# Kernel optimization log

Hardware: AMD Instinct MI355X
Metric: run time of the kernel (lower is better)

The kernel has to match this reference:

```python
import jax, jax.numpy as jnp
import numpy as np

FACTOR = 2  # StyleGAN upsample factor
K1D = jnp.array([1.0, 4.0, 6.0, 4.0, 1.0], dtype=jnp.float32)
# StyleGAN upfirdn padding for upsample: p = kw - factor = 3
# pad0 = (p+1)//2 + factor - 1 = 3 ; pad1 = p//2 = 1 (+1 extra trailing zero
# because lhs_dilation gives length 2D-1 while zero-insertion gives 2D)
PAD0, PAD1 = 3, 2


def _upfir_axis(x, k1d, axis):
    """Zero-insert (factor 2) + 5-tap FIR along one spatial axis, depthwise.

    x: [N, C, D, H, W]; axis in {2, 3, 4}.
    """
    C = x.shape[1]
    kshape = [1, 1, 1]
    kshape[axis - 2] = k1d.shape[0]
    kernel = jnp.broadcast_to(k1d.reshape(kshape), (C, 1) + tuple(kshape))
    dil = [1, 1, 1]
    dil[axis - 2] = FACTOR
    pad = [(0, 0)] * 3
    pad[axis - 2] = (PAD0, PAD1)
    return jax.lax.conv_general_dilated(
        x, kernel.astype(x.dtype),
        window_strides=(1, 1, 1), padding=pad, lhs_dilation=dil,
        dimension_numbers=('NCDHW', 'OIDHW', 'NCDHW'),
        feature_group_count=C)


def setup_inputs() -> dict:
    key = jax.random.key(0)
    x = jax.random.normal(key, (4, 32, 48, 48, 48), dtype=jnp.float32)
    return {"x": x}


def reference(x):
    # normalize so kernel sums to 1, then apply gain factor per axis so the
    # total gain is factor**3 (StyleGAN: k = k/sum(k) * gain * factor**ndim,
    # split evenly across the 3 separable passes -> factor per axis)
    k = (K1D / K1D.sum() * FACTOR).astype(x.dtype)
    for ax in (2, 3, 4):  # D, H, W
        x = _upfir_axis(x, k, ax)
    return x  # [N, C, 2D, 2H, 2W]
```

## Files before the change

### kernel.cpp

```cpp
#include <hip/hip_runtime.h>


#define IN_D 48
#define IN_H 48
#define IN_W 48
#define NC   128
#define TD   8
#define THI  8
#define NTX  24
#define NTY  16
#define NTHREADS (NTX * NTY)
#define LZ (TD + 2)
#define LY (THI + 2)
#define LXP 52
#define NROWS (LZ * LY)

__device__ __forceinline__ float4 f4_even(float4 a, float4 b) {
    return make_float4(0.5f * (a.x + b.x), 0.5f * (a.y + b.y),
                       0.5f * (a.z + b.z), 0.5f * (a.w + b.w));
}
__device__ __forceinline__ float4 f4_odd(float4 a, float4 b, float4 c) {
    return make_float4(0.125f * (a.x + c.x) + 0.75f * b.x,
                       0.125f * (a.y + c.y) + 0.75f * b.y,
                       0.125f * (a.z + c.z) + 0.75f * b.z,
                       0.125f * (a.w + c.w) + 0.75f * b.w);
}

__global__ __launch_bounds__(NTHREADS)
void upfir3d_kernel(const float* __restrict__ in,
                    float* __restrict__ out) {
    __shared__ float lds[NROWS * LXP];

    const int tx = threadIdx.x;
    const int ty = threadIdx.y;
    const int bh = blockIdx.x;
    const int dz = blockIdx.y;
    const int nc = blockIdx.z;

    const int ih0 = bh * THI;
    const int id0 = dz * TD;
    const float* inb = in + (size_t)nc * (IN_D * IN_H * IN_W);

    const int tid = ty * NTX + tx;

    if (tid < 2 * NROWS) {
        int row = tid >> 1;
        int col = (tid & 1) ? 49 : 0;
        lds[row * LXP + col] = 0.0f;
    }

    {
        const int q = tid % 12;
        for (int row = tid / 12; row < NROWS; row += NTHREADS / 12) {
            int z  = row / LY;
            int y  = row - z * LY;
            int gd = id0 - 1 + z;
            int gh = ih0 - 1 + y;
            float4 v = make_float4(0.f, 0.f, 0.f, 0.f);
            if ((unsigned)gd < (unsigned)IN_D && (unsigned)gh < (unsigned)IN_H) {
                v = *reinterpret_cast<const float4*>(
                        inb + ((size_t)gd * IN_H + gh) * IN_W + 4 * q);
            }
            float* dst = &lds[row * LXP + 1 + 4 * q];
            dst[0] = v.x; dst[1] = v.y; dst[2] = v.z; dst[3] = v.w;
        }
    }
    __syncthreads();

    const int p   = ty & 1;
    const float wga = p ? 0.125f : 0.5f;
    const float wgb = p ? 0.75f  : 0.5f;
    const float wgc = p ? 0.125f : 0.0f;
    const int yy0 = ty >> 1;
    const int cx  = 2 * tx;

    auto whpart = [&](int z) -> float4 {
        const float* pp = &lds[(z * LY + yy0) * LXP + cx];
        float4 q4 = make_float4(0.f, 0.f, 0.f, 0.f);
#pragma unroll
        for (int dy = 0; dy < 3; ++dy) {
            const float wt = (dy == 0) ? wga : (dy == 1) ? wgb : wgc;
            float2 a = *reinterpret_cast<const float2*>(pp + dy * LXP);
            float2 b = *reinterpret_cast<const float2*>(pp + dy * LXP + 2);
            float w0 = 0.5f   * (a.x + a.y);
            float w1 = 0.125f * (a.x + b.x) + 0.75f * a.y;
            float w2 = 0.5f   * (a.y + b.x);
            float w3 = 0.125f * (a.y + b.y) + 0.75f * b.x;
            q4.x += wt * w0; q4.y += wt * w1;
            q4.z += wt * w2; q4.w += wt * w3;
        }
        return q4;
    };

    float4 qm = whpart(0);
    float4 qc = whpart(1);

    const int OH = 2 * IN_H, OW = 2 * IN_W;
    const int orow = 2 * ih0 + ty;
    float* ob = out + (size_t)nc * (2 * IN_D * OH * OW)
                    + (size_t)orow * OW + 4 * tx;
    const size_t plane = (size_t)OH * OW;

#pragma unroll
    for (int d = 0; d < TD; ++d) {
        float4 qp = whpart(d + 2);
        const int od = 2 * (id0 + d);

        *reinterpret_cast<float4*>(ob + (size_t)od * plane)       = f4_even(qm, qc);
        *reinterpret_cast<float4*>(ob + (size_t)(od + 1) * plane) = f4_odd(qm, qc, qp);

        qm = qc;
        qc = qp;
    }
}

extern "C" void kernel_launch(void* const* d_in, const int* in_sizes, int n_in,
                              void* d_out, int out_size, void* d_ws, size_t ws_size,
                              hipStream_t stream) {
    const float* x = (const float*)d_in[0];
    float* out = (float*)d_out;

    dim3 grid(IN_H / THI, IN_D / TD, NC);
    dim3 block(NTX, NTY, 1);
    upfir3d_kernel<<<grid, block, 0, stream>>>(x, out);
}
```

Measured before the change: 480.5 us.

## Tile full H extent per block with register-blocked rows and shallower depth tile

Each block now covers the full 48-row H extent and a 4-deep D slab, instead of an 8x8 H-by-D tile. Each thread computes 6 row groups held in register arrays, and the H halo rows are no longer reloaded by neighbouring blocks. The grid shrinks to 12x128 blocks, the LDS footprint grows to about 62KB, and register pressure rises. Output addressing moves to 32-bit unsigned offsets, which cuts address arithmetic but relies on per-batch offsets fitting in 32 bits.

```diff
diff --git a/kernel.cpp b/kernel.cpp
--- a/kernel.cpp
+++ b/kernel.cpp
@@ -5,15 +5,16 @@
 #define IN_H 48
 #define IN_W 48
 #define NC   128
-#define TD   8
-#define THI  8
+#define TD   4
 #define NTX  24
 #define NTY  16
 #define NTHREADS (NTX * NTY)
-#define LZ (TD + 2)
-#define LY (THI + 2)
+#define LZ  (TD + 2)
+#define LYS 50
 #define LXP 52
-#define NROWS (LZ * LY)
+#define NR  6
+#define OWD 96
+#define PLANE (96 * 96)
 
 __device__ __forceinline__ float4 f4_even(float4 a, float4 b) {
     return make_float4(0.5f * (a.x + b.x), 0.5f * (a.y + b.y),
@@ -29,88 +30,95 @@
 __global__ __launch_bounds__(NTHREADS)
 void upfir3d_kernel(const float* __restrict__ in,
                     float* __restrict__ out) {
-    __shared__ float lds[NROWS * LXP];
+    __shared__ float lds[LZ * LYS * LXP];
 
     const int tx = threadIdx.x;
     const int ty = threadIdx.y;
-    const int bh = blockIdx.x;
-    const int dz = blockIdx.y;
-    const int nc = blockIdx.z;
-
-    const int ih0 = bh * THI;
+    const int dz = blockIdx.x;
+    const int nc = blockIdx.y;
     const int id0 = dz * TD;
     const float* inb = in + (size_t)nc * (IN_D * IN_H * IN_W);
-
     const int tid = ty * NTX + tx;
 
-    if (tid < 2 * NROWS) {
-        int row = tid >> 1;
-        int col = (tid & 1) ? 49 : 0;
-        lds[row * LXP + col] = 0.0f;
+    for (int idx = tid; idx < LZ * 2 * LXP; idx += NTHREADS) {
+        int z   = idx / (2 * LXP);
+        int rem = idx - z * (2 * LXP);
+        int y   = (rem < LXP) ? 0 : (LYS - 1);
+        int col = (rem < LXP) ? rem : rem - LXP;
+        lds[(z * LYS + y) * LXP + col] = 0.0f;
     }
-
-    {
-        const int q = tid % 12;
-        for (int row = tid / 12; row < NROWS; row += NTHREADS / 12) {
-            int z  = row / LY;
-            int y  = row - z * LY;
-            int gd = id0 - 1 + z;
-            int gh = ih0 - 1 + y;
-            float4 v = make_float4(0.f, 0.f, 0.f, 0.f);
-            if ((unsigned)gd < (unsigned)IN_D && (unsigned)gh < (unsigned)IN_H) {
-                v = *reinterpret_cast<const float4*>(
-                        inb + ((size_t)gd * IN_H + gh) * IN_W + 4 * q);
-            }
-            float* dst = &lds[row * LXP + 1 + 4 * q];
-            dst[0] = v.x; dst[1] = v.y; dst[2] = v.z; dst[3] = v.w;
-        }
+    for (int idx = tid; idx < LZ * IN_H * 2; idx += NTHREADS) {
+        int z   = idx / (IN_H * 2);
+        int rem = idx - z * (IN_H * 2);
+        int y   = 1 + (rem >> 1);
+        int col = (rem & 1) ? 49 : 0;
+        lds[(z * LYS + y) * LXP + col] = 0.0f;
+    }
+    for (int idx = tid; idx < LZ * IN_H * 12; idx += NTHREADS) {
+        int q  = idx % 12;
+        int rf = idx / 12;
+        int z  = rf / IN_H;
+        int y  = rf - z * IN_H;
+        int gd = id0 - 1 + z;
+        float4 v = make_float4(0.f, 0.f, 0.f, 0.f);
+        if ((unsigned)gd < (unsigned)IN_D)
+            v = *reinterpret_cast<const float4*>(
+                    inb + ((size_t)gd * IN_H + y) * IN_W + 4 * q);
+        float* dst = &lds[(z * LYS + 1 + y) * LXP + 1 + 4 * q];
+        dst[0] = v.x; dst[1] = v.y; dst[2] = v.z; dst[3] = v.w;
     }
     __syncthreads();
 
-    const int p   = ty & 1;
+    const int p = ty & 1;
     const float wga = p ? 0.125f : 0.5f;
     const float wgb = p ? 0.75f  : 0.5f;
     const float wgc = p ? 0.125f : 0.0f;
-    const int yy0 = ty >> 1;
-    const int cx  = 2 * tx;
+    const int yb = ty >> 1;
+    const int cx = 2 * tx;
 
-    auto whpart = [&](int z) -> float4 {
-        const float* pp = &lds[(z * LY + yy0) * LXP + cx];
+    auto whpart = [&](int z, int r) -> float4 {
+        const float* pp = &lds[(z * LYS + yb + 8 * r) * LXP + cx];
         float4 q4 = make_float4(0.f, 0.f, 0.f, 0.f);
 #pragma unroll
         for (int dy = 0; dy < 3; ++dy) {
             const float wt = (dy == 0) ? wga : (dy == 1) ? wgb : wgc;
             float2 a = *reinterpret_cast<const float2*>(pp + dy * LXP);
             float2 b = *reinterpret_cast<const float2*>(pp + dy * LXP + 2);
-            float w0 = 0.5f   * (a.x + a.y);
-            float w1 = 0.125f * (a.x + b.x) + 0.75f * a.y;
-            float w2 = 0.5f   * (a.y + b.x);
-            float w3 = 0.125f * (a.y + b.y) + 0.75f * b.x;
-            q4.x += wt * w0; q4.y += wt * w1;
-            q4.z += wt * w2; q4.w += wt * w3;
+            q4.x += wt * (0.5f   * (a.x + a.y));
+            q4.y += wt * (0.125f * (a.x + b.x) + 0.75f * a.y);
+            q4.z += wt * (0.5f   * (a.y + b.x));
+            q4.w += wt * (0.125f * (a.y + b.y) + 0.75f * b.x);
         }
         return q4;
     };
 
-    float4 qm = whpart(0);
-    float4 qc = whpart(1);
+    float4 qm[NR], qc[NR];
+#pragma unroll
+    for (int r = 0; r < NR; ++r) qm[r] = whpart(0, r);
+#pragma unroll
+    for (int r = 0; r < NR; ++r) qc[r] = whpart(1, r);
 
-    const int OH = 2 * IN_H, OW = 2 * IN_W;
-    const int orow = 2 * ih0 + ty;
-    float* ob = out + (size_t)nc * (2 * IN_D * OH * OW)
-                    + (size_t)orow * OW + 4 * tx;
-    const size_t plane = (size_t)OH * OW;
+    float* ob = out + (size_t)nc * (96 * PLANE);
+    const unsigned robase = (unsigned)(ty * OWD + 4 * tx);
 
 #pragma unroll
     for (int d = 0; d < TD; ++d) {
-        float4 qp = whpart(d + 2);
-        const int od = 2 * (id0 + d);
+        float4 qp[NR];
+#pragma unroll
+        for (int r = 0; r < NR; ++r) qp[r] = whpart(d + 2, r);
 
-        *reinterpret_cast<float4*>(ob + (size_t)od * plane)       = f4_even(qm, qc);
-        *reinterpret_cast<float4*>(ob + (size_t)(od + 1) * plane) = f4_odd(qm, qc, qp);
+        const unsigned pe = (unsigned)((8 * dz + 2 * d) * PLANE);
+#pragma unroll
+        for (int r = 0; r < NR; ++r)
+            *reinterpret_cast<float4*>(ob + pe + robase + 1536u * r)
+                = f4_even(qm[r], qc[r]);
+#pragma unroll
+        for (int r = 0; r < NR; ++r)
+            *reinterpret_cast<float4*>(ob + pe + PLANE + robase + 1536u * r)
+                = f4_odd(qm[r], qc[r], qp[r]);
 
-        qm = qc;
-        qc = qp;
+#pragma unroll
+        for (int r = 0; r < NR; ++r) { qm[r] = qc[r]; qc[r] = qp[r]; }
     }
 }
 
@@ -120,7 +128,7 @@
     const float* x = (const float*)d_in[0];
     float* out = (float*)d_out;
 
-    dim3 grid(IN_H / THI, IN_D / TD, NC);
+    dim3 grid(IN_D / TD, NC, 1);
     dim3 block(NTX, NTY, 1);
     upfir3d_kernel<<<grid, block, 0, stream>>>(x, out);
 }
```

After: 500.2 us. 4.1% more time.
